# Kernel tuning notes

Measured on AMD Instinct MI355X. Metric: run time of the kernel, lower is better.

Reference implementation:

```python
import jax, jax.numpy as jnp
import numpy as np

N_NODES = 50000
N_EDGES = 640000
HID = 128
EDGE_FEAT = 4
NUM_G = 20
R_MIN, R_MAX = 0.0, 10.0

def setup_inputs() -> dict:
    key = jax.random.key(0)
    ks = jax.random.split(key, 16)
    s = lambda d: 1.0 / np.sqrt(d)
    return {
        'h': jax.random.normal(ks[0], (N_NODES, HID), jnp.float32),
        'x': jax.random.normal(ks[1], (N_NODES, 3), jnp.float32),
        'edge_index': jax.random.randint(ks[2], (2, N_EDGES), 0, N_NODES, dtype=jnp.int64),
        'mask_ligand': jnp.ones((N_NODES,), jnp.float32),
        'edge_attr': jax.random.normal(ks[3], (N_EDGES, EDGE_FEAT), jnp.float32),
        'We1': jax.random.normal(ks[4], (2*HID+EDGE_FEAT+NUM_G, HID), jnp.float32) * s(2*HID+EDGE_FEAT+NUM_G),
        'be1': jnp.zeros((HID,), jnp.float32),
        'We2': jax.random.normal(ks[5], (HID, HID), jnp.float32) * s(HID),
        'be2': jnp.zeros((HID,), jnp.float32),
        'Winf': jax.random.normal(ks[6], (HID, 1), jnp.float32) * s(HID),
        'binf': jnp.zeros((1,), jnp.float32),
        'Wx1': jax.random.normal(ks[7], (HID, HID), jnp.float32) * s(HID),
        'bx1': jnp.zeros((HID,), jnp.float32),
        'Wx2': jax.random.normal(ks[8], (HID, 1), jnp.float32) * 0.001 * s(HID),
        'Wn1': jax.random.normal(ks[9], (2*HID, HID), jnp.float32) * s(2*HID),
        'bn1': jnp.zeros((HID,), jnp.float32),
        'Wn2': jax.random.normal(ks[10], (HID, HID), jnp.float32) * s(HID),
        'bn2': jnp.zeros((HID,), jnp.float32),
    }

def reference(h, x, edge_index, mask_ligand, edge_attr,
              We1, be1, We2, be2, Winf, binf, Wx1, bx1, Wx2, Wn1, bn1, Wn2, bn2):
    n = h.shape[0]
    src, dst = edge_index[0], edge_index[1]
    hi, hj = h[dst], h[src]                      # [E, H] gathers
    rel_x = x[dst] - x[src]                      # [E, 3]
    d_sq = jnp.sum(rel_x**2, axis=-1, keepdims=True)  # [E, 1]
    d = jnp.sqrt(d_sq + 1e-8)
    # GaussianSmearing(r_min=0, r_max=10, num_gaussians=20)
    offset = jnp.linspace(R_MIN, R_MAX, NUM_G, dtype=h.dtype)
    coeff = -0.5 / (offset[1] - offset[0])**2
    d_feat = jnp.exp(coeff * (d - offset)**2)    # [E, 20]
    edge_feat = jnp.concatenate([d_feat, edge_attr], axis=-1)
    # edge MLP (2 layers, silu, act_last=True)
    z = jnp.concatenate([hi, hj, edge_feat], axis=-1)
    mij = jax.nn.silu(jax.nn.silu(z @ We1 + be1) @ We2 + be2)  # [E, H]
    eij = jax.nn.sigmoid(mij @ Winf + binf)      # [E, 1]
    mi = jax.ops.segment_sum(mij * eij, dst, num_segments=n)   # [N, H]
    # node MLP (2 layers, silu, no act on last)
    nz = jnp.concatenate([mi, h], axis=-1)
    h_out = h + (jax.nn.silu(nz @ Wn1 + bn1) @ Wn2 + bn2)
    # coordinate update
    xg = jnp.tanh(jax.nn.silu(mij @ Wx1 + bx1) @ Wx2)          # [E, 1]
    delta_x = jax.ops.segment_sum(rel_x / (d + 1.0) * xg, dst, num_segments=n)
    x_out = x + delta_x * mask_ligand[:, None]
    return h_out, x_out
```

## Files before the change

### kernel.cpp

```cpp
#include <hip/hip_runtime.h>
#include <math.h>

#define NN 50000
#define NE 640000
#define H 128
#define EPB 32
#define NPB 32
#define ZB 296
#define BB 136
#define KP1 288
#define NZB 264

typedef __attribute__((ext_vector_type(8))) unsigned short u16x8;
typedef __attribute__((ext_vector_type(8))) __bf16 bf16x8;
typedef __attribute__((ext_vector_type(2))) __bf16 bf16x2;
typedef __attribute__((ext_vector_type(4))) float f32x4;

__device__ __forceinline__ float frcp(float x) {
#if __has_builtin(__builtin_amdgcn_rcpf)
    return __builtin_amdgcn_rcpf(x);
#else
    return 1.0f / x;
#endif
}

__device__ __forceinline__ float silu_f(float v) {
    return v * frcp(1.0f + __expf(-v));
}

__device__ __forceinline__ float sigmoid_f(float v) {
    return frcp(1.0f + __expf(-v));
}

__device__ __forceinline__ float tanh_f(float v) {
    return 1.0f - 2.0f * frcp(1.0f + __expf(2.0f * v));
}

__device__ __forceinline__ unsigned short f2bf(float f) {
    unsigned int u = __builtin_bit_cast(unsigned int, f);
    u += 0x7FFFu + ((u >> 16) & 1u);
    return (unsigned short)(u >> 16);
}

__device__ __forceinline__ float bf2f(unsigned short s) {
    unsigned int u = ((unsigned int)s) << 16;
    return __builtin_bit_cast(float, u);
}

__device__ __forceinline__ unsigned int pkbf(float lo, float hi) {
#if __has_builtin(__builtin_amdgcn_cvt_pk_bf16_f32)
    bf16x2 v = __builtin_amdgcn_cvt_pk_bf16_f32(lo, hi);
    unsigned int r; __builtin_memcpy(&r, &v, 4); return r;
#else
    return (unsigned int)f2bf(lo) | ((unsigned int)f2bf(hi) << 16);
#endif
}

__device__ __forceinline__ f32x4 mfma16(u16x8 a, u16x8 b, f32x4 c) {
    return __builtin_amdgcn_mfma_f32_16x16x32_bf16(
        __builtin_bit_cast(bf16x8, a), __builtin_bit_cast(bf16x8, b), c, 0, 0, 0);
}

template<int KT, int INSTR, bool SYNC_BEFORE_EPI>
__device__ __forceinline__ void layer_mfma(
    const unsigned short* __restrict__ inbuf,
    const unsigned short* __restrict__ wt,
    const float* __restrict__ bias,
    unsigned short* __restrict__ outbuf,
    int wv, int quad, int r16)
{
    f32x4 acc[2][2] = {};
    const int F = wv * 32;
    #pragma unroll
    for (int ks = 0; ks < KT / 32; ks++) {
        int ko = ks * 32 + quad * 8;
        u16x8 b0 = *(const u16x8*)(inbuf + r16 * INSTR + ko);
        u16x8 b1 = *(const u16x8*)(inbuf + (16 + r16) * INSTR + ko);
        u16x8 a0 = *(const u16x8*)(wt + (size_t)(F + r16) * KT + ko);
        u16x8 a1 = *(const u16x8*)(wt + (size_t)(F + 16 + r16) * KT + ko);
        acc[0][0] = mfma16(a0, b0, acc[0][0]);
        acc[0][1] = mfma16(a0, b1, acc[0][1]);
        acc[1][0] = mfma16(a1, b0, acc[1][0]);
        acc[1][1] = mfma16(a1, b1, acc[1][1]);
    }
    if (SYNC_BEFORE_EPI) __syncthreads();
    #pragma unroll
    for (int rt = 0; rt < 2; rt++) {
        int f0 = F + rt * 16 + quad * 4;
        float4 bv = *(const float4*)(bias + f0);
        #pragma unroll
        for (int ci = 0; ci < 2; ci++) {
            int e = ci * 16 + r16;
            float s0 = silu_f(acc[rt][ci][0] + bv.x);
            float s1 = silu_f(acc[rt][ci][1] + bv.y);
            float s2 = silu_f(acc[rt][ci][2] + bv.z);
            float s3 = silu_f(acc[rt][ci][3] + bv.w);
            uint2 p = { pkbf(s0, s1), pkbf(s2, s3) };
            *(uint2*)(outbuf + e * BB + f0) = p;
        }
    }
}

__global__ __launch_bounds__(256) void convert_weights(
    const float* __restrict__ We1, const float* __restrict__ We2,
    const float* __restrict__ Wx1, const float* __restrict__ Wn1,
    const float* __restrict__ Wn2,
    unsigned short* __restrict__ w1t, unsigned short* __restrict__ w2t,
    unsigned short* __restrict__ wx1t, unsigned short* __restrict__ wn1t,
    unsigned short* __restrict__ wn2t)
{
    int i = blockIdx.x * 256 + threadIdx.x;
    const int S1 = 128 * KP1;
    const int S2 = 128 * 128;
    const int S3 = 128 * 256;
    if (i < S1) {
        int n = i / KP1, k = i % KP1;
        w1t[i] = (k < 280) ? f2bf(We1[k * H + n]) : (unsigned short)0;
    } else if (i < S1 + S2) {
        int j = i - S1; int n = j / H, k = j % H;
        w2t[j] = f2bf(We2[k * H + n]);
    } else if (i < S1 + 2 * S2) {
        int j = i - S1 - S2; int n = j / H, k = j % H;
        wx1t[j] = f2bf(Wx1[k * H + n]);
    } else if (i < S1 + 2 * S2 + S3) {
        int j = i - S1 - 2 * S2; int n = j / 256, k = j % 256;
        wn1t[j] = f2bf(Wn1[k * H + n]);
    } else if (i < S1 + 3 * S2 + S3) {
        int j = i - S1 - 2 * S2 - S3; int n = j / H, k = j % H;
        wn2t[j] = f2bf(Wn2[k * H + n]);
    }
}

__global__ __launch_bounds__(256) void zero_kernel(float4* __restrict__ p, int n4) {
    int i = blockIdx.x * 256 + threadIdx.x;
    if (i < n4) p[i] = make_float4(0.f, 0.f, 0.f, 0.f);
}

__global__ __launch_bounds__(256, 7) void edge_kernel(
    const float* __restrict__ h, const float* __restrict__ x,
    const int* __restrict__ ei, const float* __restrict__ edge_attr,
    const unsigned short* __restrict__ w1t, const float* __restrict__ be1,
    const unsigned short* __restrict__ w2t, const float* __restrict__ be2,
    const float* __restrict__ Winf, const float* __restrict__ binf,
    const unsigned short* __restrict__ wx1t, const float* __restrict__ bx1,
    const float* __restrict__ Wx2,
    float* __restrict__ mi, float* __restrict__ dx)
{
    __shared__ unsigned short zs[EPB * ZB];
    __shared__ float relx_s[EPB][3];
    __shared__ float eij_s[EPB];
    __shared__ float epart[4][EPB];
    __shared__ float xpart[4][EPB];
    __shared__ int dst_s[EPB];
    __shared__ float winf_s[H];
    __shared__ float wx2_s[H];

    unsigned short* m1 = zs;
    unsigned short* m2 = zs + EPB * BB;

    const int t = threadIdx.x;
    const int e0 = blockIdx.x * EPB;

    if (t >= 128 && t < 256) {
        winf_s[t - 128] = Winf[t - 128];
        wx2_s[t - 128] = Wx2[t - 128];
    }

    {
        int e = t >> 3, l = t & 7;
        int s = ei[e0 + e], d = ei[NE + e0 + e];
        const float4* hd = (const float4*)(h + (size_t)d * H);
        const float4* hs = (const float4*)(h + (size_t)s * H);
        unsigned short* zr = zs + e * ZB;
        float4 v0 = hd[l * 4 + 0], v1 = hd[l * 4 + 1];
        float4 v2 = hd[l * 4 + 2], v3 = hd[l * 4 + 3];
        uint4 p0 = { pkbf(v0.x, v0.y), pkbf(v0.z, v0.w), pkbf(v1.x, v1.y), pkbf(v1.z, v1.w) };
        uint4 p1 = { pkbf(v2.x, v2.y), pkbf(v2.z, v2.w), pkbf(v3.x, v3.y), pkbf(v3.z, v3.w) };
        *(uint4*)(zr + l * 16) = p0;
        *(uint4*)(zr + l * 16 + 8) = p1;
        float4 w0 = hs[l * 4 + 0], w1 = hs[l * 4 + 1];
        float4 w2 = hs[l * 4 + 2], w3 = hs[l * 4 + 3];
        uint4 q0 = { pkbf(w0.x, w0.y), pkbf(w0.z, w0.w), pkbf(w1.x, w1.y), pkbf(w1.z, w1.w) };
        uint4 q1 = { pkbf(w2.x, w2.y), pkbf(w2.z, w2.w), pkbf(w3.x, w3.y), pkbf(w3.z, w3.w) };
        *(uint4*)(zr + 128 + l * 16) = q0;
        *(uint4*)(zr + 128 + l * 16 + 8) = q1;
    }
    if (t < EPB) {
        int s = ei[e0 + t], d = ei[NE + e0 + t];
        dst_s[t] = d;
        float rx = x[d * 3 + 0] - x[s * 3 + 0];
        float ry = x[d * 3 + 1] - x[s * 3 + 1];
        float rz = x[d * 3 + 2] - x[s * 3 + 2];
        float d2 = rx * rx + ry * ry + rz * rz;
        float dd = sqrtf(d2 + 1e-8f);
        float inv = frcp(dd + 1.0f);
        relx_s[t][0] = rx * inv;
        relx_s[t][1] = ry * inv;
        relx_s[t][2] = rz * inv;
        const float step = 10.0f / 19.0f;
        const float coeff = -0.5f / (step * step);
        unsigned short* zr = zs + t * ZB;
        #pragma unroll
        for (int g = 0; g < 20; g++) {
            float df = dd - step * (float)g;
            zr[256 + g] = f2bf(__expf(coeff * df * df));
        }
        #pragma unroll
        for (int j = 0; j < 4; j++)
            zr[276 + j] = f2bf(edge_attr[(size_t)(e0 + t) * 4 + j]);
        #pragma unroll
        for (int j = 280; j < ZB; j++) zr[j] = 0;
    }
    __syncthreads();

    const int wv = t >> 6, lane = t & 63;
    const int quad = lane >> 4, r16 = lane & 15;
    const int F = wv * 32;

    layer_mfma<KP1, ZB, true>(zs, w1t, be1, m1, wv, quad, r16);
    __syncthreads();

    {
        f32x4 acc[2][2] = {};
        #pragma unroll
        for (int ks = 0; ks < H / 32; ks++) {
            int ko = ks * 32 + quad * 8;
            u16x8 b0 = *(const u16x8*)(m1 + r16 * BB + ko);
            u16x8 b1 = *(const u16x8*)(m1 + (16 + r16) * BB + ko);
            u16x8 a0 = *(const u16x8*)(w2t + (size_t)(F + r16) * H + ko);
            u16x8 a1 = *(const u16x8*)(w2t + (size_t)(F + 16 + r16) * H + ko);
            acc[0][0] = mfma16(a0, b0, acc[0][0]);
            acc[0][1] = mfma16(a0, b1, acc[0][1]);
            acc[1][0] = mfma16(a1, b0, acc[1][0]);
            acc[1][1] = mfma16(a1, b1, acc[1][1]);
        }
        float ep[2] = {0.f, 0.f};
        #pragma unroll
        for (int rt = 0; rt < 2; rt++) {
            int f0 = F + rt * 16 + quad * 4;
            float4 bv = *(const float4*)(be2 + f0);
            float4 wf = *(const float4*)(winf_s + f0);
            #pragma unroll
            for (int ci = 0; ci < 2; ci++) {
                int e = ci * 16 + r16;
                float s0 = silu_f(acc[rt][ci][0] + bv.x);
                float s1 = silu_f(acc[rt][ci][1] + bv.y);
                float s2 = silu_f(acc[rt][ci][2] + bv.z);
                float s3 = silu_f(acc[rt][ci][3] + bv.w);
                ep[ci] += s0 * wf.x + s1 * wf.y + s2 * wf.z + s3 * wf.w;
                uint2 p = { pkbf(s0, s1), pkbf(s2, s3) };
                *(uint2*)(m2 + e * BB + f0) = p;
            }
        }
        #pragma unroll
        for (int ci = 0; ci < 2; ci++) {
            ep[ci] += __shfl_xor(ep[ci], 16, 64);
            ep[ci] += __shfl_xor(ep[ci], 32, 64);
        }
        if (quad == 0) {
            epart[wv][r16] = ep[0];
            epart[wv][16 + r16] = ep[1];
        }
    }
    __syncthreads();

    if (t < EPB) {
        float s = epart[0][t] + epart[1][t] + epart[2][t] + epart[3][t] + binf[0];
        eij_s[t] = sigmoid_f(s);
    }

    {
        f32x4 acc[2][2] = {};
        #pragma unroll
        for (int ks = 0; ks < H / 32; ks++) {
            int ko = ks * 32 + quad * 8;
            u16x8 b0 = *(const u16x8*)(m2 + r16 * BB + ko);
            u16x8 b1 = *(const u16x8*)(m2 + (16 + r16) * BB + ko);
            u16x8 a0 = *(const u16x8*)(wx1t + (size_t)(F + r16) * H + ko);
            u16x8 a1 = *(const u16x8*)(wx1t + (size_t)(F + 16 + r16) * H + ko);
            acc[0][0] = mfma16(a0, b0, acc[0][0]);
            acc[0][1] = mfma16(a0, b1, acc[0][1]);
            acc[1][0] = mfma16(a1, b0, acc[1][0]);
            acc[1][1] = mfma16(a1, b1, acc[1][1]);
        }
        float xp[2] = {0.f, 0.f};
        #pragma unroll
        for (int rt = 0; rt < 2; rt++) {
            int f0 = F + rt * 16 + quad * 4;
            float4 bv = *(const float4*)(bx1 + f0);
            float4 wf = *(const float4*)(wx2_s + f0);
            #pragma unroll
            for (int ci = 0; ci < 2; ci++) {
                xp[ci] += silu_f(acc[rt][ci][0] + bv.x) * wf.x
                        + silu_f(acc[rt][ci][1] + bv.y) * wf.y
                        + silu_f(acc[rt][ci][2] + bv.z) * wf.z
                        + silu_f(acc[rt][ci][3] + bv.w) * wf.w;
            }
        }
        #pragma unroll
        for (int ci = 0; ci < 2; ci++) {
            xp[ci] += __shfl_xor(xp[ci], 16, 64);
            xp[ci] += __shfl_xor(xp[ci], 32, 64);
        }
        if (quad == 0) {
            xpart[wv][r16] = xp[0];
            xpart[wv][16 + r16] = xp[1];
        }
    }
    __syncthreads();

    {
        int k = t & 127, eh = t >> 7;
        for (int e = eh; e < EPB; e += 2) {
            float mv = bf2f(m2[e * BB + k]) * eij_s[e];
            atomicAdd(&mi[(size_t)dst_s[e] * H + k], mv);
        }
        if (t < EPB * 3) {
            int e = t / 3, dim = t % 3;
            float xs = xpart[0][e] + xpart[1][e] + xpart[2][e] + xpart[3][e];
            float xg = tanh_f(xs);
            atomicAdd(&dx[(size_t)dst_s[e] * 3 + dim], relx_s[e][dim] * xg);
        }
    }
}

__global__ __launch_bounds__(256, 8) void node_kernel(
    const float* __restrict__ h, const float* __restrict__ x,
    const float* __restrict__ mask,
    const unsigned short* __restrict__ wn1t, const float* __restrict__ bn1,
    const unsigned short* __restrict__ wn2t, const float* __restrict__ bn2,
    float* __restrict__ mi_hout, float* __restrict__ dx_xout)
{
    __shared__ unsigned short nzs[NPB * NZB];

    unsigned short* nbuf = nzs;

    const int t = threadIdx.x;
    const int n0 = blockIdx.x * NPB;

    {
        int r = t >> 3, l = t & 7;
        int n = n0 + r;
        unsigned short* zr = nzs + r * NZB;
        if (n < NN) {
            const float4* mi4 = (const float4*)(mi_hout + (size_t)n * H);
            const float4* h4  = (const float4*)(h + (size_t)n * H);
            float4 v0 = mi4[l * 4 + 0], v1 = mi4[l * 4 + 1];
            float4 v2 = mi4[l * 4 + 2], v3 = mi4[l * 4 + 3];
            uint4 p0 = { pkbf(v0.x, v0.y), pkbf(v0.z, v0.w), pkbf(v1.x, v1.y), pkbf(v1.z, v1.w) };
            uint4 p1 = { pkbf(v2.x, v2.y), pkbf(v2.z, v2.w), pkbf(v3.x, v3.y), pkbf(v3.z, v3.w) };
            *(uint4*)(zr + l * 16) = p0;
            *(uint4*)(zr + l * 16 + 8) = p1;
            float4 w0 = h4[l * 4 + 0], w1 = h4[l * 4 + 1];
            float4 w2 = h4[l * 4 + 2], w3 = h4[l * 4 + 3];
            uint4 q0 = { pkbf(w0.x, w0.y), pkbf(w0.z, w0.w), pkbf(w1.x, w1.y), pkbf(w1.z, w1.w) };
            uint4 q1 = { pkbf(w2.x, w2.y), pkbf(w2.z, w2.w), pkbf(w3.x, w3.y), pkbf(w3.z, w3.w) };
            *(uint4*)(zr + 128 + l * 16) = q0;
            *(uint4*)(zr + 128 + l * 16 + 8) = q1;
        } else {
            uint4 zf = {0u, 0u, 0u, 0u};
            *(uint4*)(zr + l * 16) = zf;
            *(uint4*)(zr + l * 16 + 8) = zf;
            *(uint4*)(zr + 128 + l * 16) = zf;
            *(uint4*)(zr + 128 + l * 16 + 8) = zf;
        }
    }

    float xo = 0.f;
    int xn = -1, xdim = 0;
    if (t < NPB * 3) {
        int r = t / 3; xdim = t % 3;
        int n = n0 + r;
        if (n < NN) {
            xn = n;
            xo = x[(size_t)n * 3 + xdim] + dx_xout[(size_t)n * 3 + xdim] * mask[n];
        }
    }
    __syncthreads();

    if (xn >= 0) dx_xout[(size_t)xn * 3 + xdim] = xo;

    const int wv = t >> 6, lane = t & 63;
    const int quad = lane >> 4, r16 = lane & 15;

    layer_mfma<2 * H, NZB, true>(nzs, wn1t, bn1, nbuf, wv, quad, r16);
    __syncthreads();

    {
        f32x4 acc[2][2] = {};
        const int F = wv * 32;
        #pragma unroll
        for (int ks = 0; ks < H / 32; ks++) {
            int ko = ks * 32 + quad * 8;
            u16x8 b0 = *(const u16x8*)(nbuf + r16 * BB + ko);
            u16x8 b1 = *(const u16x8*)(nbuf + (16 + r16) * BB + ko);
            u16x8 a0 = *(const u16x8*)(wn2t + (size_t)(F + r16) * H + ko);
            u16x8 a1 = *(const u16x8*)(wn2t + (size_t)(F + 16 + r16) * H + ko);
            acc[0][0] = mfma16(a0, b0, acc[0][0]);
            acc[0][1] = mfma16(a0, b1, acc[0][1]);
            acc[1][0] = mfma16(a1, b0, acc[1][0]);
            acc[1][1] = mfma16(a1, b1, acc[1][1]);
        }
        #pragma unroll
        for (int rt = 0; rt < 2; rt++) {
            int f0 = F + rt * 16 + quad * 4;
            float4 bv = *(const float4*)(bn2 + f0);
            #pragma unroll
            for (int ci = 0; ci < 2; ci++) {
                int n = n0 + ci * 16 + r16;
                if (n < NN) {
                    float4 hv = *(const float4*)(h + (size_t)n * H + f0);
                    float4 o;
                    o.x = hv.x + acc[rt][ci][0] + bv.x;
                    o.y = hv.y + acc[rt][ci][1] + bv.y;
                    o.z = hv.z + acc[rt][ci][2] + bv.z;
                    o.w = hv.w + acc[rt][ci][3] + bv.w;
                    *(float4*)(mi_hout + (size_t)n * H + f0) = o;
                }
            }
        }
    }
}

extern "C" void kernel_launch(void* const* d_in, const int* in_sizes, int n_in,
                              void* d_out, int out_size, void* d_ws, size_t ws_size,
                              hipStream_t stream) {
    const float* h     = (const float*)d_in[0];
    const float* x     = (const float*)d_in[1];
    const int*   ei    = (const int*)d_in[2];
    const float* mask  = (const float*)d_in[3];
    const float* eattr = (const float*)d_in[4];
    const float* We1   = (const float*)d_in[5];
    const float* be1   = (const float*)d_in[6];
    const float* We2   = (const float*)d_in[7];
    const float* be2   = (const float*)d_in[8];
    const float* Winf  = (const float*)d_in[9];
    const float* binf  = (const float*)d_in[10];
    const float* Wx1   = (const float*)d_in[11];
    const float* bx1   = (const float*)d_in[12];
    const float* Wx2   = (const float*)d_in[13];
    const float* Wn1   = (const float*)d_in[14];
    const float* bn1   = (const float*)d_in[15];
    const float* Wn2   = (const float*)d_in[16];
    const float* bn2   = (const float*)d_in[17];

    float* mi = (float*)d_out;
    float* dx = mi + (size_t)NN * H;

    unsigned short* w1t  = (unsigned short*)d_ws;
    unsigned short* w2t  = w1t + 128 * KP1;
    unsigned short* wx1t = w2t + 128 * H;
    unsigned short* wn1t = wx1t + 128 * H;
    unsigned short* wn2t = wn1t + 128 * 256;

    const int wconv_total = 128 * KP1 + 3 * 128 * H + 128 * 256;
    convert_weights<<<(wconv_total + 255) / 256, 256, 0, stream>>>(
        We1, We2, Wx1, Wn1, Wn2, w1t, w2t, wx1t, wn1t, wn2t);

    const int total4 = (NN * H + NN * 3) / 4;
    zero_kernel<<<(total4 + 255) / 256, 256, 0, stream>>>((float4*)d_out, total4);

    edge_kernel<<<NE / EPB, 256, 0, stream>>>(
        h, x, ei, eattr, w1t, be1, w2t, be2, Winf, binf, wx1t, bx1, Wx2, mi, dx);

    node_kernel<<<(NN + NPB - 1) / NPB, 256, 0, stream>>>(
        h, x, mask, wn1t, bn1, wn2t, bn2, mi, dx);
}
```

Before: 522.2 us.

## Replace atomic mi scatter with CSR gather and pre-converted bf16 h

Builds a CSR of edges by destination (histogram, single-block scan, scatter). The edge kernel now writes eij-scaled messages in bf16 per edge instead of doing 128 float atomics per edge. The node kernel then gathers and sums each node's incoming messages, which removes the float atomic traffic on mi and the zeroing of the large output. It also pre-converts h to bf16 once so the edge gathers read half the bytes. The cost is extra kernels, a serial single-block scan, a 164MB bf16 intermediate write/read, bf16 precision in the message sum, and reliance on a large enough workspace.

```diff
diff --git a/kernel.cpp b/kernel.cpp
--- a/kernel.cpp
+++ b/kernel.cpp
@@ -10,6 +10,8 @@
 #define BB 136
 #define KP1 288
 #define NZB 264
+#define SCAN_T 1024
+#define CHUNK 49
 
 typedef __attribute__((ext_vector_type(8))) unsigned short u16x8;
 typedef __attribute__((ext_vector_type(8))) __bf16 bf16x8;
@@ -24,17 +26,9 @@
 #endif
 }
 
-__device__ __forceinline__ float silu_f(float v) {
-    return v * frcp(1.0f + __expf(-v));
-}
-
-__device__ __forceinline__ float sigmoid_f(float v) {
-    return frcp(1.0f + __expf(-v));
-}
-
-__device__ __forceinline__ float tanh_f(float v) {
-    return 1.0f - 2.0f * frcp(1.0f + __expf(2.0f * v));
-}
+__device__ __forceinline__ float silu_f(float v) { return v * frcp(1.0f + __expf(-v)); }
+__device__ __forceinline__ float sigmoid_f(float v) { return frcp(1.0f + __expf(-v)); }
+__device__ __forceinline__ float tanh_f(float v) { return 1.0f - 2.0f * frcp(1.0f + __expf(2.0f * v)); }
 
 __device__ __forceinline__ unsigned short f2bf(float f) {
     unsigned int u = __builtin_bit_cast(unsigned int, f);
@@ -131,12 +125,373 @@
     }
 }
 
+__global__ __launch_bounds__(256) void hconv_kernel(
+    const float* __restrict__ h, unsigned short* __restrict__ h2)
+{
+    int i = blockIdx.x * 256 + threadIdx.x;
+    if (i < NN * H / 8) {
+        const float4* p = (const float4*)(h) + i * 2;
+        float4 a = p[0], b = p[1];
+        uint4 o = { pkbf(a.x, a.y), pkbf(a.z, a.w), pkbf(b.x, b.y), pkbf(b.z, b.w) };
+        *(uint4*)(h2 + (size_t)i * 8) = o;
+    }
+}
+
 __global__ __launch_bounds__(256) void zero_kernel(float4* __restrict__ p, int n4) {
     int i = blockIdx.x * 256 + threadIdx.x;
     if (i < n4) p[i] = make_float4(0.f, 0.f, 0.f, 0.f);
 }
 
-__global__ __launch_bounds__(256, 7) void edge_kernel(
+__global__ __launch_bounds__(256) void zero_ints(int* __restrict__ p, int n) {
+    int i = blockIdx.x * 256 + threadIdx.x;
+    if (i < n) p[i] = 0;
+}
+
+__global__ __launch_bounds__(256) void hist_kernel(
+    const int* __restrict__ ei, int* __restrict__ cnt)
+{
+    int e = blockIdx.x * 256 + threadIdx.x;
+    if (e < NE) atomicAdd(&cnt[ei[NE + e]], 1);
+}
+
+__global__ __launch_bounds__(SCAN_T) void scan_kernel(
+    int* __restrict__ cnt, int* __restrict__ rowptr)
+{
+    __shared__ int part[SCAN_T];
+    int t = threadIdx.x;
+    int beg = t * CHUNK, end = min(beg + CHUNK, NN);
+    int s = 0;
+    for (int i = beg; i < end; i++) s += cnt[i];
+    part[t] = s;
+    __syncthreads();
+    for (int off = 1; off < SCAN_T; off <<= 1) {
+        int v = (t >= off) ? part[t - off] : 0;
+        __syncthreads();
+        part[t] += v;
+        __syncthreads();
+    }
+    int run = (t == 0) ? 0 : part[t - 1];
+    for (int i = beg; i < end; i++) {
+        int c = cnt[i];
+        rowptr[i] = run;
+        cnt[i] = run;
+        run += c;
+    }
+    if (t == 0) rowptr[NN] = NE;
+}
+
+__global__ __launch_bounds__(256) void scatter_kernel(
+    const int* __restrict__ ei, int* __restrict__ cursor, int* __restrict__ eidx)
+{
+    int e = blockIdx.x * 256 + threadIdx.x;
+    if (e < NE) {
+        int d = ei[NE + e];
+        int pos = atomicAdd(&cursor[d], 1);
+        eidx[pos] = e;
+    }
+}
+
+__global__ __launch_bounds__(256, 7) void edge_kernel_csr(
+    const unsigned short* __restrict__ h2, const float* __restrict__ x,
+    const int* __restrict__ ei, const float* __restrict__ edge_attr,
+    const unsigned short* __restrict__ w1t, const float* __restrict__ be1,
+    const unsigned short* __restrict__ w2t, const float* __restrict__ be2,
+    const float* __restrict__ Winf, const float* __restrict__ binf,
+    const unsigned short* __restrict__ wx1t, const float* __restrict__ bx1,
+    const float* __restrict__ Wx2,
+    unsigned short* __restrict__ mijE, float* __restrict__ dx)
+{
+    __shared__ unsigned short zs[EPB * ZB];
+    __shared__ float relx_s[EPB][3];
+    __shared__ float eij_s[EPB];
+    __shared__ float epart[4][EPB];
+    __shared__ float xpart[4][EPB];
+    __shared__ int dst_s[EPB];
+    __shared__ float winf_s[H];
+    __shared__ float wx2_s[H];
+
+    unsigned short* m1 = zs;
+    unsigned short* m2 = zs + EPB * BB;
+
+    const int t = threadIdx.x;
+    const int e0 = blockIdx.x * EPB;
+
+    if (t >= 128 && t < 256) {
+        winf_s[t - 128] = Winf[t - 128];
+        wx2_s[t - 128] = Wx2[t - 128];
+    }
+
+    {
+        int e = t >> 3, l = t & 7;
+        int s = ei[e0 + e], d = ei[NE + e0 + e];
+        const uint4* hd = (const uint4*)(h2 + (size_t)d * H);
+        const uint4* hs = (const uint4*)(h2 + (size_t)s * H);
+        unsigned short* zr = zs + e * ZB;
+        *(uint4*)(zr + l * 16)           = hd[l * 2];
+        *(uint4*)(zr + l * 16 + 8)       = hd[l * 2 + 1];
+        *(uint4*)(zr + 128 + l * 16)     = hs[l * 2];
+        *(uint4*)(zr + 128 + l * 16 + 8) = hs[l * 2 + 1];
+    }
+    if (t < EPB) {
+        int s = ei[e0 + t], d = ei[NE + e0 + t];
+        dst_s[t] = d;
+        float rx = x[d * 3 + 0] - x[s * 3 + 0];
+        float ry = x[d * 3 + 1] - x[s * 3 + 1];
+        float rz = x[d * 3 + 2] - x[s * 3 + 2];
+        float d2 = rx * rx + ry * ry + rz * rz;
+        float dd = sqrtf(d2 + 1e-8f);
+        float inv = frcp(dd + 1.0f);
+        relx_s[t][0] = rx * inv;
+        relx_s[t][1] = ry * inv;
+        relx_s[t][2] = rz * inv;
+        const float step = 10.0f / 19.0f;
+        const float coeff = -0.5f / (step * step);
+        unsigned short* zr = zs + t * ZB;
+        #pragma unroll
+        for (int g = 0; g < 20; g++) {
+            float df = dd - step * (float)g;
+            zr[256 + g] = f2bf(__expf(coeff * df * df));
+        }
+        #pragma unroll
+        for (int j = 0; j < 4; j++)
+            zr[276 + j] = f2bf(edge_attr[(size_t)(e0 + t) * 4 + j]);
+        #pragma unroll
+        for (int j = 280; j < ZB; j++) zr[j] = 0;
+    }
+    __syncthreads();
+
+    const int wv = t >> 6, lane = t & 63;
+    const int quad = lane >> 4, r16 = lane & 15;
+    const int F = wv * 32;
+
+    layer_mfma<KP1, ZB, true>(zs, w1t, be1, m1, wv, quad, r16);
+    __syncthreads();
+
+    {
+        f32x4 acc[2][2] = {};
+        #pragma unroll
+        for (int ks = 0; ks < H / 32; ks++) {
+            int ko = ks * 32 + quad * 8;
+            u16x8 b0 = *(const u16x8*)(m1 + r16 * BB + ko);
+            u16x8 b1 = *(const u16x8*)(m1 + (16 + r16) * BB + ko);
+            u16x8 a0 = *(const u16x8*)(w2t + (size_t)(F + r16) * H + ko);
+            u16x8 a1 = *(const u16x8*)(w2t + (size_t)(F + 16 + r16) * H + ko);
+            acc[0][0] = mfma16(a0, b0, acc[0][0]);
+            acc[0][1] = mfma16(a0, b1, acc[0][1]);
+            acc[1][0] = mfma16(a1, b0, acc[1][0]);
+            acc[1][1] = mfma16(a1, b1, acc[1][1]);
+        }
+        float ep[2] = {0.f, 0.f};
+        #pragma unroll
+        for (int rt = 0; rt < 2; rt++) {
+            int f0 = F + rt * 16 + quad * 4;
+            float4 bv = *(const float4*)(be2 + f0);
+            float4 wf = *(const float4*)(winf_s + f0);
+            #pragma unroll
+            for (int ci = 0; ci < 2; ci++) {
+                int e = ci * 16 + r16;
+                float s0 = silu_f(acc[rt][ci][0] + bv.x);
+                float s1 = silu_f(acc[rt][ci][1] + bv.y);
+                float s2 = silu_f(acc[rt][ci][2] + bv.z);
+                float s3 = silu_f(acc[rt][ci][3] + bv.w);
+                ep[ci] += s0 * wf.x + s1 * wf.y + s2 * wf.z + s3 * wf.w;
+                uint2 p = { pkbf(s0, s1), pkbf(s2, s3) };
+                *(uint2*)(m2 + e * BB + f0) = p;
+            }
+        }
+        #pragma unroll
+        for (int ci = 0; ci < 2; ci++) {
+            ep[ci] += __shfl_xor(ep[ci], 16, 64);
+            ep[ci] += __shfl_xor(ep[ci], 32, 64);
+        }
+        if (quad == 0) {
+            epart[wv][r16] = ep[0];
+            epart[wv][16 + r16] = ep[1];
+        }
+    }
+    __syncthreads();
+
+    if (t < EPB) {
+        float s = epart[0][t] + epart[1][t] + epart[2][t] + epart[3][t] + binf[0];
+        eij_s[t] = sigmoid_f(s);
+    }
+
+    {
+        f32x4 acc[2][2] = {};
+        #pragma unroll
+        for (int ks = 0; ks < H / 32; ks++) {
+            int ko = ks * 32 + quad * 8;
+            u16x8 b0 = *(const u16x8*)(m2 + r16 * BB + ko);
+            u16x8 b1 = *(const u16x8*)(m2 + (16 + r16) * BB + ko);
+            u16x8 a0 = *(const u16x8*)(wx1t + (size_t)(F + r16) * H + ko);
+            u16x8 a1 = *(const u16x8*)(wx1t + (size_t)(F + 16 + r16) * H + ko);
+            acc[0][0] = mfma16(a0, b0, acc[0][0]);
+            acc[0][1] = mfma16(a0, b1, acc[0][1]);
+            acc[1][0] = mfma16(a1, b0, acc[1][0]);
+            acc[1][1] = mfma16(a1, b1, acc[1][1]);
+        }
+        float xp[2] = {0.f, 0.f};
+        #pragma unroll
+        for (int rt = 0; rt < 2; rt++) {
+            int f0 = F + rt * 16 + quad * 4;
+            float4 bv = *(const float4*)(bx1 + f0);
+            float4 wf = *(const float4*)(wx2_s + f0);
+            #pragma unroll
+            for (int ci = 0; ci < 2; ci++) {
+                xp[ci] += silu_f(acc[rt][ci][0] + bv.x) * wf.x
+                        + silu_f(acc[rt][ci][1] + bv.y) * wf.y
+                        + silu_f(acc[rt][ci][2] + bv.z) * wf.z
+                        + silu_f(acc[rt][ci][3] + bv.w) * wf.w;
+            }
+        }
+        #pragma unroll
+        for (int ci = 0; ci < 2; ci++) {
+            xp[ci] += __shfl_xor(xp[ci], 16, 64);
+            xp[ci] += __shfl_xor(xp[ci], 32, 64);
+        }
+        if (quad == 0) {
+            xpart[wv][r16] = xp[0];
+            xpart[wv][16 + r16] = xp[1];
+        }
+    }
+    __syncthreads();
+
+    {
+        int e = t >> 3, l = t & 7;
+        float eij = eij_s[e];
+        const unsigned short* row = m2 + e * BB + l * 16;
+        u16x8 v0 = *(const u16x8*)(row);
+        u16x8 v1 = *(const u16x8*)(row + 8);
+        uint4 o0, o1;
+        o0.x = pkbf(bf2f(v0[0]) * eij, bf2f(v0[1]) * eij);
+        o0.y = pkbf(bf2f(v0[2]) * eij, bf2f(v0[3]) * eij);
+        o0.z = pkbf(bf2f(v0[4]) * eij, bf2f(v0[5]) * eij);
+        o0.w = pkbf(bf2f(v0[6]) * eij, bf2f(v0[7]) * eij);
+        o1.x = pkbf(bf2f(v1[0]) * eij, bf2f(v1[1]) * eij);
+        o1.y = pkbf(bf2f(v1[2]) * eij, bf2f(v1[3]) * eij);
+        o1.z = pkbf(bf2f(v1[4]) * eij, bf2f(v1[5]) * eij);
+        o1.w = pkbf(bf2f(v1[6]) * eij, bf2f(v1[7]) * eij);
+        uint4* dst = (uint4*)(mijE + (size_t)(e0 + e) * H + l * 16);
+        dst[0] = o0;
+        dst[1] = o1;
+    }
+    if (t < EPB * 3) {
+        int e = t / 3, dim = t % 3;
+        float xs = xpart[0][e] + xpart[1][e] + xpart[2][e] + xpart[3][e];
+        float xg = tanh_f(xs);
+        atomicAdd(&dx[(size_t)dst_s[e] * 3 + dim], relx_s[e][dim] * xg);
+    }
+}
+
+__global__ __launch_bounds__(256, 6) void node_kernel_csr(
+    const unsigned short* __restrict__ h2, const float* __restrict__ h,
+    const float* __restrict__ x, const float* __restrict__ mask,
+    const int* __restrict__ rowptr, const int* __restrict__ eidx,
+    const unsigned short* __restrict__ mijE,
+    const unsigned short* __restrict__ wn1t, const float* __restrict__ bn1,
+    const unsigned short* __restrict__ wn2t, const float* __restrict__ bn2,
+    float* __restrict__ hout, float* __restrict__ dx_xout)
+{
+    __shared__ unsigned short nzs[NPB * NZB];
+    unsigned short* nbuf = nzs;
+
+    const int t = threadIdx.x;
+    const int n0 = blockIdx.x * NPB;
+
+    {
+        int r = t >> 3, l = t & 7;
+        int n = n0 + r;
+        float av[16];
+        #pragma unroll
+        for (int k = 0; k < 16; k++) av[k] = 0.f;
+        if (n < NN) {
+            int beg = rowptr[n], end = rowptr[n + 1];
+            for (int j = beg; j < end; j++) {
+                int e = eidx[j];
+                const u16x8* p = (const u16x8*)(mijE + (size_t)e * H + l * 16);
+                u16x8 a = p[0], b = p[1];
+                #pragma unroll
+                for (int k = 0; k < 8; k++) {
+                    av[k]     += bf2f(a[k]);
+                    av[8 + k] += bf2f(b[k]);
+                }
+            }
+        }
+        unsigned short* zr = nzs + r * NZB;
+        uint4 pa = { pkbf(av[0], av[1]), pkbf(av[2], av[3]),
+                     pkbf(av[4], av[5]), pkbf(av[6], av[7]) };
+        uint4 pb = { pkbf(av[8], av[9]), pkbf(av[10], av[11]),
+                     pkbf(av[12], av[13]), pkbf(av[14], av[15]) };
+        *(uint4*)(zr + l * 16)     = pa;
+        *(uint4*)(zr + l * 16 + 8) = pb;
+        if (n < NN) {
+            const uint4* hp = (const uint4*)(h2 + (size_t)n * H);
+            *(uint4*)(zr + 128 + l * 16)     = hp[l * 2];
+            *(uint4*)(zr + 128 + l * 16 + 8) = hp[l * 2 + 1];
+        } else {
+            uint4 zf = {0u, 0u, 0u, 0u};
+            *(uint4*)(zr + 128 + l * 16)     = zf;
+            *(uint4*)(zr + 128 + l * 16 + 8) = zf;
+        }
+    }
+
+    float xo = 0.f;
+    int xn = -1, xdim = 0;
+    if (t < NPB * 3) {
+        int r = t / 3; xdim = t % 3;
+        int n = n0 + r;
+        if (n < NN) {
+            xn = n;
+            xo = x[(size_t)n * 3 + xdim] + dx_xout[(size_t)n * 3 + xdim] * mask[n];
+        }
+    }
+    __syncthreads();
+
+    if (xn >= 0) dx_xout[(size_t)xn * 3 + xdim] = xo;
+
+    const int wv = t >> 6, lane = t & 63;
+    const int quad = lane >> 4, r16 = lane & 15;
+
+    layer_mfma<2 * H, NZB, true>(nzs, wn1t, bn1, nbuf, wv, quad, r16);
+    __syncthreads();
+
+    {
+        f32x4 acc[2][2] = {};
+        const int F = wv * 32;
+        #pragma unroll
+        for (int ks = 0; ks < H / 32; ks++) {
+            int ko = ks * 32 + quad * 8;
+            u16x8 b0 = *(const u16x8*)(nbuf + r16 * BB + ko);
+            u16x8 b1 = *(const u16x8*)(nbuf + (16 + r16) * BB + ko);
+            u16x8 a0 = *(const u16x8*)(wn2t + (size_t)(F + r16) * H + ko);
+            u16x8 a1 = *(const u16x8*)(wn2t + (size_t)(F + 16 + r16) * H + ko);
+            acc[0][0] = mfma16(a0, b0, acc[0][0]);
+            acc[0][1] = mfma16(a0, b1, acc[0][1]);
+            acc[1][0] = mfma16(a1, b0, acc[1][0]);
+            acc[1][1] = mfma16(a1, b1, acc[1][1]);
+        }
+        #pragma unroll
+        for (int rt = 0; rt < 2; rt++) {
+            int f0 = F + rt * 16 + quad * 4;
+            float4 bv = *(const float4*)(bn2 + f0);
+            #pragma unroll
+            for (int ci = 0; ci < 2; ci++) {
+                int n = n0 + ci * 16 + r16;
+                if (n < NN) {
+                    float4 hv = *(const float4*)(h + (size_t)n * H + f0);
+                    float4 o;
+                    o.x = hv.x + acc[rt][ci][0] + bv.x;
+                    o.y = hv.y + acc[rt][ci][1] + bv.y;
+                    o.z = hv.z + acc[rt][ci][2] + bv.z;
+                    o.w = hv.w + acc[rt][ci][3] + bv.w;
+                    *(float4*)(hout + (size_t)n * H + f0) = o;
+                }
+            }
+        }
+    }
+}
+
+__global__ __launch_bounds__(256, 7) void edge_kernel_atomic(
     const float* __restrict__ h, const float* __restrict__ x,
     const int* __restrict__ ei, const float* __restrict__ edge_attr,
     const unsigned short* __restrict__ w1t, const float* __restrict__ be1,
@@ -165,7 +520,6 @@
         winf_s[t - 128] = Winf[t - 128];
         wx2_s[t - 128] = Wx2[t - 128];
     }
-
     {
         int e = t >> 3, l = t & 7;
         int s = ei[e0 + e], d = ei[NE + e0 + e];
@@ -268,7 +622,6 @@
         float s = epart[0][t] + epart[1][t] + epart[2][t] + epart[3][t] + binf[0];
         eij_s[t] = sigmoid_f(s);
     }
-
     {
         f32x4 acc[2][2] = {};
         #pragma unroll
@@ -324,7 +677,7 @@
     }
 }
 
-__global__ __launch_bounds__(256, 8) void node_kernel(
+__global__ __launch_bounds__(256, 8) void node_kernel_atomic(
     const float* __restrict__ h, const float* __restrict__ x,
     const float* __restrict__ mask,
     const unsigned short* __restrict__ wn1t, const float* __restrict__ bn1,
@@ -332,7 +685,6 @@
     float* __restrict__ mi_hout, float* __restrict__ dx_xout)
 {
     __shared__ unsigned short nzs[NPB * NZB];
-
     unsigned short* nbuf = nzs;
 
     const int t = threadIdx.x;
@@ -444,25 +796,50 @@
     const float* Wn2   = (const float*)d_in[16];
     const float* bn2   = (const float*)d_in[17];
 
-    float* mi = (float*)d_out;
-    float* dx = mi + (size_t)NN * H;
-
+    float* hout = (float*)d_out;
+    float* dx   = hout + (size_t)NN * H;
+
+    const size_t W_SH = 128 * KP1 + 3 * 128 * H + 128 * 256;
     unsigned short* w1t  = (unsigned short*)d_ws;
     unsigned short* w2t  = w1t + 128 * KP1;
     unsigned short* wx1t = w2t + 128 * H;
     unsigned short* wn1t = wx1t + 128 * H;
     unsigned short* wn2t = wn1t + 128 * 256;
-
-    const int wconv_total = 128 * KP1 + 3 * 128 * H + 128 * 256;
+    unsigned short* h2   = wn2t + 128 * H;
+    int* cnt    = (int*)(h2 + (size_t)NN * H);
+    int* rowptr = cnt + NN;
+    int* eidx   = rowptr + NN + 1;
+    unsigned short* mijE = (unsigned short*)(eidx + NE);
+    size_t need = (char*)(mijE + (size_t)NE * H) - (char*)d_ws;
+    const bool use_csr = ws_size >= need;
+
+    const int wconv_total = (int)W_SH;
     convert_weights<<<(wconv_total + 255) / 256, 256, 0, stream>>>(
         We1, We2, Wx1, Wn1, Wn2, w1t, w2t, wx1t, wn1t, wn2t);
 
-    const int total4 = (NN * H + NN * 3) / 4;
-    zero_kernel<<<(total4 + 255) / 256, 256, 0, stream>>>((float4*)d_out, total4);
-
-    edge_kernel<<<NE / EPB, 256, 0, stream>>>(
-        h, x, ei, eattr, w1t, be1, w2t, be2, Winf, binf, wx1t, bx1, Wx2, mi, dx);
-
-    node_kernel<<<(NN + NPB - 1) / NPB, 256, 0, stream>>>(
-        h, x, mask, wn1t, bn1, wn2t, bn2, mi, dx);
-}
+    if (use_csr) {
+        hconv_kernel<<<(NN * H / 8 + 255) / 256, 256, 0, stream>>>(h, h2);
+        zero_ints<<<(NN + 255) / 256, 256, 0, stream>>>(cnt, NN);
+        zero_kernel<<<(NN * 3 / 4 + 255) / 256, 256, 0, stream>>>((float4*)dx, NN * 3 / 4);
+        hist_kernel<<<(NE + 255) / 256, 256, 0, stream>>>(ei, cnt);
+        scan_kernel<<<1, SCAN_T, 0, stream>>>(cnt, rowptr);
+        scatter_kernel<<<(NE + 255) / 256, 256, 0, stream>>>(ei, cnt, eidx);
+
+        edge_kernel_csr<<<NE / EPB, 256, 0, stream>>>(
+            h2, x, ei, eattr, w1t, be1, w2t, be2, Winf, binf, wx1t, bx1, Wx2,
+            mijE, dx);
+
+        node_kernel_csr<<<(NN + NPB - 1) / NPB, 256, 0, stream>>>(
+            h2, h, x, mask, rowptr, eidx, mijE, wn1t, bn1, wn2t, bn2, hout, dx);
+    } else {
+        const int total4 = (NN * H + NN * 3) / 4;
+        zero_kernel<<<(total4 + 255) / 256, 256, 0, stream>>>((float4*)d_out, total4);
+
+        edge_kernel_atomic<<<NE / EPB, 256, 0, stream>>>(
+            h, x, ei, eattr, w1t, be1, w2t, be2, Winf, binf, wx1t, bx1, Wx2,
+            hout, dx);
+
+        node_kernel_atomic<<<(NN + NPB - 1) / NPB, 256, 0, stream>>>(
+            h, x, mask, wn1t, bn1, wn2t, bn2, hout, dx);
+    }
+}
```

After: 646.1 us. 1.24x slower.

## Replace atomic message scatter with CSR dst-sorted edges and gather-sum in node kernel

Applied to the files above, without the earlier changes.

Builds a CSR by destination each call (histogram, single-block scan, atomic scatter of edge ids). The edge kernel processes edges in dst-sorted order and writes eij-scaled messages as bf16 per edge instead of doing fp32 atomicAdds into mi. The node kernel then sums each node's message rows. h is also pre-converted to bf16 once, which halves gather traffic. This removes 82M float atomics but adds several small kernels, a serial-ish scan, and an extra 164MB bf16 message write and read, with bf16 rounding on per-edge messages.

```diff
diff --git a/kernel.cpp b/kernel.cpp
--- a/kernel.cpp
+++ b/kernel.cpp
@@ -10,6 +10,8 @@
 #define BB 136
 #define KP1 288
 #define NZB 264
+#define SCAN_T 1024
+#define CHUNK 49
 
 typedef __attribute__((ext_vector_type(8))) unsigned short u16x8;
 typedef __attribute__((ext_vector_type(8))) __bf16 bf16x8;
@@ -24,17 +26,9 @@
 #endif
 }
 
-__device__ __forceinline__ float silu_f(float v) {
-    return v * frcp(1.0f + __expf(-v));
-}
-
-__device__ __forceinline__ float sigmoid_f(float v) {
-    return frcp(1.0f + __expf(-v));
-}
-
-__device__ __forceinline__ float tanh_f(float v) {
-    return 1.0f - 2.0f * frcp(1.0f + __expf(2.0f * v));
-}
+__device__ __forceinline__ float silu_f(float v) { return v * frcp(1.0f + __expf(-v)); }
+__device__ __forceinline__ float sigmoid_f(float v) { return frcp(1.0f + __expf(-v)); }
+__device__ __forceinline__ float tanh_f(float v) { return 1.0f - 2.0f * frcp(1.0f + __expf(2.0f * v)); }
 
 __device__ __forceinline__ unsigned short f2bf(float f) {
     unsigned int u = __builtin_bit_cast(unsigned int, f);
@@ -131,20 +125,82 @@
     }
 }
 
+__global__ __launch_bounds__(256) void hconv_kernel(
+    const float* __restrict__ h, unsigned short* __restrict__ h2)
+{
+    int i = blockIdx.x * 256 + threadIdx.x;
+    if (i < NN * H / 8) {
+        const float4* p = (const float4*)(h) + i * 2;
+        float4 a = p[0], b = p[1];
+        uint4 o = { pkbf(a.x, a.y), pkbf(a.z, a.w), pkbf(b.x, b.y), pkbf(b.z, b.w) };
+        *(uint4*)(h2 + (size_t)i * 8) = o;
+    }
+}
+
 __global__ __launch_bounds__(256) void zero_kernel(float4* __restrict__ p, int n4) {
     int i = blockIdx.x * 256 + threadIdx.x;
     if (i < n4) p[i] = make_float4(0.f, 0.f, 0.f, 0.f);
 }
 
-__global__ __launch_bounds__(256, 7) void edge_kernel(
-    const float* __restrict__ h, const float* __restrict__ x,
+__global__ __launch_bounds__(256) void zero_ints(int* __restrict__ p, int n) {
+    int i = blockIdx.x * 256 + threadIdx.x;
+    if (i < n) p[i] = 0;
+}
+
+__global__ __launch_bounds__(256) void hist_kernel(
+    const int* __restrict__ ei, int* __restrict__ cnt)
+{
+    int e = blockIdx.x * 256 + threadIdx.x;
+    if (e < NE) atomicAdd(&cnt[ei[NE + e]], 1);
+}
+
+__global__ __launch_bounds__(SCAN_T) void scan_kernel(
+    int* __restrict__ cnt, int* __restrict__ rowptr)
+{
+    __shared__ int part[SCAN_T];
+    int t = threadIdx.x;
+    int beg = t * CHUNK, end = min(beg + CHUNK, NN);
+    int s = 0;
+    for (int i = beg; i < end; i++) s += cnt[i];
+    part[t] = s;
+    __syncthreads();
+    for (int off = 1; off < SCAN_T; off <<= 1) {
+        int v = (t >= off) ? part[t - off] : 0;
+        __syncthreads();
+        part[t] += v;
+        __syncthreads();
+    }
+    int run = (t == 0) ? 0 : part[t - 1];
+    for (int i = beg; i < end; i++) {
+        int c = cnt[i];
+        rowptr[i] = run;
+        cnt[i] = run;
+        run += c;
+    }
+    if (t == 0) rowptr[NN] = NE;
+}
+
+__global__ __launch_bounds__(256) void scatter_kernel(
+    const int* __restrict__ ei, int* __restrict__ cursor, int* __restrict__ eidx)
+{
+    int e = blockIdx.x * 256 + threadIdx.x;
+    if (e < NE) {
+        int d = ei[NE + e];
+        int pos = atomicAdd(&cursor[d], 1);
+        eidx[pos] = e;
+    }
+}
+
+__global__ __launch_bounds__(256, 7) void edge_kernel_csr(
+    const unsigned short* __restrict__ h2, const float* __restrict__ x,
     const int* __restrict__ ei, const float* __restrict__ edge_attr,
+    const int* __restrict__ eidx,
     const unsigned short* __restrict__ w1t, const float* __restrict__ be1,
     const unsigned short* __restrict__ w2t, const float* __restrict__ be2,
     const float* __restrict__ Winf, const float* __restrict__ binf,
     const unsigned short* __restrict__ wx1t, const float* __restrict__ bx1,
     const float* __restrict__ Wx2,
-    float* __restrict__ mi, float* __restrict__ dx)
+    unsigned short* __restrict__ mijE, float* __restrict__ dx)
 {
     __shared__ unsigned short zs[EPB * ZB];
     __shared__ float relx_s[EPB][3];
@@ -168,25 +224,19 @@
 
     {
         int e = t >> 3, l = t & 7;
-        int s = ei[e0 + e], d = ei[NE + e0 + e];
-        const float4* hd = (const float4*)(h + (size_t)d * H);
-        const float4* hs = (const float4*)(h + (size_t)s * H);
+        int eo = eidx[e0 + e];
+        int s = ei[eo], d = ei[NE + eo];
+        const uint4* hd = (const uint4*)(h2 + (size_t)d * H);
+        const uint4* hs = (const uint4*)(h2 + (size_t)s * H);
         unsigned short* zr = zs + e * ZB;
-        float4 v0 = hd[l * 4 + 0], v1 = hd[l * 4 + 1];
-        float4 v2 = hd[l * 4 + 2], v3 = hd[l * 4 + 3];
-        uint4 p0 = { pkbf(v0.x, v0.y), pkbf(v0.z, v0.w), pkbf(v1.x, v1.y), pkbf(v1.z, v1.w) };
-        uint4 p1 = { pkbf(v2.x, v2.y), pkbf(v2.z, v2.w), pkbf(v3.x, v3.y), pkbf(v3.z, v3.w) };
-        *(uint4*)(zr + l * 16) = p0;
-        *(uint4*)(zr + l * 16 + 8) = p1;
-        float4 w0 = hs[l * 4 + 0], w1 = hs[l * 4 + 1];
-        float4 w2 = hs[l * 4 + 2], w3 = hs[l * 4 + 3];
-        uint4 q0 = { pkbf(w0.x, w0.y), pkbf(w0.z, w0.w), pkbf(w1.x, w1.y), pkbf(w1.z, w1.w) };
-        uint4 q1 = { pkbf(w2.x, w2.y), pkbf(w2.z, w2.w), pkbf(w3.x, w3.y), pkbf(w3.z, w3.w) };
-        *(uint4*)(zr + 128 + l * 16) = q0;
-        *(uint4*)(zr + 128 + l * 16 + 8) = q1;
+        *(uint4*)(zr + l * 16)           = hd[l * 2];
+        *(uint4*)(zr + l * 16 + 8)       = hd[l * 2 + 1];
+        *(uint4*)(zr + 128 + l * 16)     = hs[l * 2];
+        *(uint4*)(zr + 128 + l * 16 + 8) = hs[l * 2 + 1];
     }
     if (t < EPB) {
-        int s = ei[e0 + t], d = ei[NE + e0 + t];
+        int eo = eidx[e0 + t];
+        int s = ei[eo], d = ei[NE + eo];
         dst_s[t] = d;
         float rx = x[d * 3 + 0] - x[s * 3 + 0];
         float ry = x[d * 3 + 1] - x[s * 3 + 1];
@@ -207,7 +257,7 @@
         }
         #pragma unroll
         for (int j = 0; j < 4; j++)
-            zr[276 + j] = f2bf(edge_attr[(size_t)(e0 + t) * 4 + j]);
+            zr[276 + j] = f2bf(edge_attr[(size_t)eo * 4 + j]);
         #pragma unroll
         for (int j = 280; j < ZB; j++) zr[j] = 0;
     }
@@ -310,29 +360,42 @@
     __syncthreads();
 
     {
-        int k = t & 127, eh = t >> 7;
-        for (int e = eh; e < EPB; e += 2) {
-            float mv = bf2f(m2[e * BB + k]) * eij_s[e];
-            atomicAdd(&mi[(size_t)dst_s[e] * H + k], mv);
-        }
-        if (t < EPB * 3) {
-            int e = t / 3, dim = t % 3;
-            float xs = xpart[0][e] + xpart[1][e] + xpart[2][e] + xpart[3][e];
-            float xg = tanh_f(xs);
-            atomicAdd(&dx[(size_t)dst_s[e] * 3 + dim], relx_s[e][dim] * xg);
-        }
-    }
-}
-
-__global__ __launch_bounds__(256, 8) void node_kernel(
-    const float* __restrict__ h, const float* __restrict__ x,
-    const float* __restrict__ mask,
+        int e = t >> 3, l = t & 7;
+        float eij = eij_s[e];
+        const unsigned short* row = m2 + e * BB + l * 16;
+        u16x8 v0 = *(const u16x8*)(row);
+        u16x8 v1 = *(const u16x8*)(row + 8);
+        uint4 o0, o1;
+        o0.x = pkbf(bf2f(v0[0]) * eij, bf2f(v0[1]) * eij);
+        o0.y = pkbf(bf2f(v0[2]) * eij, bf2f(v0[3]) * eij);
+        o0.z = pkbf(bf2f(v0[4]) * eij, bf2f(v0[5]) * eij);
+        o0.w = pkbf(bf2f(v0[6]) * eij, bf2f(v0[7]) * eij);
+        o1.x = pkbf(bf2f(v1[0]) * eij, bf2f(v1[1]) * eij);
+        o1.y = pkbf(bf2f(v1[2]) * eij, bf2f(v1[3]) * eij);
+        o1.z = pkbf(bf2f(v1[4]) * eij, bf2f(v1[5]) * eij);
+        o1.w = pkbf(bf2f(v1[6]) * eij, bf2f(v1[7]) * eij);
+        uint4* dst = (uint4*)(mijE + (size_t)(e0 + e) * H + l * 16);
+        dst[0] = o0;
+        dst[1] = o1;
+    }
+    if (t < EPB * 3) {
+        int e = t / 3, dim = t % 3;
+        float xs = xpart[0][e] + xpart[1][e] + xpart[2][e] + xpart[3][e];
+        float xg = tanh_f(xs);
+        atomicAdd(&dx[(size_t)dst_s[e] * 3 + dim], relx_s[e][dim] * xg);
+    }
+}
+
+__global__ __launch_bounds__(256, 8) void node_kernel_csr(
+    const unsigned short* __restrict__ h2, const float* __restrict__ h,
+    const float* __restrict__ x, const float* __restrict__ mask,
+    const int* __restrict__ rowptr,
+    const unsigned short* __restrict__ mijE,
     const unsigned short* __restrict__ wn1t, const float* __restrict__ bn1,
     const unsigned short* __restrict__ wn2t, const float* __restrict__ bn2,
-    float* __restrict__ mi_hout, float* __restrict__ dx_xout)
+    float* __restrict__ hout, float* __restrict__ dx_xout)
 {
     __shared__ unsigned short nzs[NPB * NZB];
-
     unsigned short* nbuf = nzs;
 
     const int t = threadIdx.x;
@@ -341,27 +404,36 @@
     {
         int r = t >> 3, l = t & 7;
         int n = n0 + r;
+        float av[16];
+        #pragma unroll
+        for (int k = 0; k < 16; k++) av[k] = 0.f;
+        if (n < NN) {
+            int beg = rowptr[n], end = rowptr[n + 1];
+            const u16x8* p = (const u16x8*)(mijE + (size_t)beg * H + l * 16);
+            for (int j = beg; j < end; j++) {
+                u16x8 a = p[0], b = p[1];
+                p += H / 8;
+                #pragma unroll
+                for (int k = 0; k < 8; k++) {
+                    av[k]     += bf2f(a[k]);
+                    av[8 + k] += bf2f(b[k]);
+                }
+            }
+        }
         unsigned short* zr = nzs + r * NZB;
+        uint4 pa = { pkbf(av[0], av[1]), pkbf(av[2], av[3]),
+                     pkbf(av[4], av[5]), pkbf(av[6], av[7]) };
+        uint4 pb = { pkbf(av[8], av[9]), pkbf(av[10], av[11]),
+                     pkbf(av[12], av[13]), pkbf(av[14], av[15]) };
+        *(uint4*)(zr + l * 16)     = pa;
+        *(uint4*)(zr + l * 16 + 8) = pb;
         if (n < NN) {
-            const float4* mi4 = (const float4*)(mi_hout + (size_t)n * H);
-            const float4* h4  = (const float4*)(h + (size_t)n * H);
-            float4 v0 = mi4[l * 4 + 0], v1 = mi4[l * 4 + 1];
-            float4 v2 = mi4[l * 4 + 2], v3 = mi4[l * 4 + 3];
-            uint4 p0 = { pkbf(v0.x, v0.y), pkbf(v0.z, v0.w), pkbf(v1.x, v1.y), pkbf(v1.z, v1.w) };
-            uint4 p1 = { pkbf(v2.x, v2.y), pkbf(v2.z, v2.w), pkbf(v3.x, v3.y), pkbf(v3.z, v3.w) };
-            *(uint4*)(zr + l * 16) = p0;
-            *(uint4*)(zr + l * 16 + 8) = p1;
-            float4 w0 = h4[l * 4 + 0], w1 = h4[l * 4 + 1];
-            float4 w2 = h4[l * 4 + 2], w3 = h4[l * 4 + 3];
-            uint4 q0 = { pkbf(w0.x, w0.y), pkbf(w0.z, w0.w), pkbf(w1.x, w1.y), pkbf(w1.z, w1.w) };
-            uint4 q1 = { pkbf(w2.x, w2.y), pkbf(w2.z, w2.w), pkbf(w3.x, w3.y), pkbf(w3.z, w3.w) };
-            *(uint4*)(zr + 128 + l * 16) = q0;
-            *(uint4*)(zr + 128 + l * 16 + 8) = q1;
+            const uint4* hp = (const uint4*)(h2 + (size_t)n * H);
+            *(uint4*)(zr + 128 + l * 16)     = hp[l * 2];
+            *(uint4*)(zr + 128 + l * 16 + 8) = hp[l * 2 + 1];
         } else {
             uint4 zf = {0u, 0u, 0u, 0u};
-            *(uint4*)(zr + l * 16) = zf;
-            *(uint4*)(zr + l * 16 + 8) = zf;
-            *(uint4*)(zr + 128 + l * 16) = zf;
+            *(uint4*)(zr + 128 + l * 16)     = zf;
             *(uint4*)(zr + 128 + l * 16 + 8) = zf;
         }
     }
@@ -415,7 +487,7 @@
                     o.y = hv.y + acc[rt][ci][1] + bv.y;
                     o.z = hv.z + acc[rt][ci][2] + bv.z;
                     o.w = hv.w + acc[rt][ci][3] + bv.w;
-                    *(float4*)(mi_hout + (size_t)n * H + f0) = o;
+                    *(float4*)(hout + (size_t)n * H + f0) = o;
                 }
             }
         }
@@ -444,25 +516,35 @@
     const float* Wn2   = (const float*)d_in[16];
     const float* bn2   = (const float*)d_in[17];
 
-    float* mi = (float*)d_out;
-    float* dx = mi + (size_t)NN * H;
-
+    float* hout = (float*)d_out;
+    float* dx   = hout + (size_t)NN * H;
+
+    const size_t W_SH = 128 * KP1 + 3 * 128 * H + 128 * 256;
     unsigned short* w1t  = (unsigned short*)d_ws;
     unsigned short* w2t  = w1t + 128 * KP1;
     unsigned short* wx1t = w2t + 128 * H;
     unsigned short* wn1t = wx1t + 128 * H;
     unsigned short* wn2t = wn1t + 128 * 256;
-
-    const int wconv_total = 128 * KP1 + 3 * 128 * H + 128 * 256;
-    convert_weights<<<(wconv_total + 255) / 256, 256, 0, stream>>>(
+    unsigned short* h2   = wn2t + 128 * H;
+    int* cnt    = (int*)(h2 + (size_t)NN * H);
+    int* rowptr = cnt + NN;
+    int* eidx   = rowptr + NN + 1;
+    unsigned short* mijE = (unsigned short*)(eidx + NE);
+
+    convert_weights<<<((int)W_SH + 255) / 256, 256, 0, stream>>>(
         We1, We2, Wx1, Wn1, Wn2, w1t, w2t, wx1t, wn1t, wn2t);
 
-    const int total4 = (NN * H + NN * 3) / 4;
-    zero_kernel<<<(total4 + 255) / 256, 256, 0, stream>>>((float4*)d_out, total4);
-
-    edge_kernel<<<NE / EPB, 256, 0, stream>>>(
-        h, x, ei, eattr, w1t, be1, w2t, be2, Winf, binf, wx1t, bx1, Wx2, mi, dx);
-
-    node_kernel<<<(NN + NPB - 1) / NPB, 256, 0, stream>>>(
-        h, x, mask, wn1t, bn1, wn2t, bn2, mi, dx);
-}
+    hconv_kernel<<<(NN * H / 8 + 255) / 256, 256, 0, stream>>>(h, h2);
+    zero_ints<<<(NN + 255) / 256, 256, 0, stream>>>(cnt, NN);
+    zero_kernel<<<(NN * 3 / 4 + 255) / 256, 256, 0, stream>>>((float4*)dx, NN * 3 / 4);
+    hist_kernel<<<(NE + 255) / 256, 256, 0, stream>>>(ei, cnt);
+    scan_kernel<<<1, SCAN_T, 0, stream>>>(cnt, rowptr);
+    scatter_kernel<<<(NE + 255) / 256, 256, 0, stream>>>(ei, cnt, eidx);
+
+    edge_kernel_csr<<<NE / EPB, 256, 0, stream>>>(
+        h2, x, ei, eattr, eidx, w1t, be1, w2t, be2, Winf, binf, wx1t, bx1, Wx2,
+        mijE, dx);
+
+    node_kernel_csr<<<(NN + NPB - 1) / NPB, 256, 0, stream>>>(
+        h2, h, x, mask, rowptr, mijE, wn1t, bn1, wn2t, bn2, hout, dx);
+}
```

Result: slower. 667.2 us (+27.8%).
